# Kernel tuning notes

Measured on AMD Instinct MI355X. Metric: run time of the kernel, lower is better.

## Reference

```python
import jax, jax.numpy as jnp
import numpy as np

B = 8192       # n_cells per batch
G = 512        # n_genes
D = 64         # expression latent dim


def setup_inputs() -> dict:
    key = jax.random.key(0)
    k1, k2 = jax.random.split(key)
    velocity = jax.random.normal(k1, (B, G), dtype=jnp.float32)
    expression_latent = jax.random.normal(k2, (B, D), dtype=jnp.float32)
    return {"velocity": velocity, "expression_latent": expression_latent}


def reference(velocity, expression_latent):
    # weighted_diff[i, j] = sum_g (v_i[g] - v_j[g])^2
    # computed via the Gram trick: ||v_i||^2 + ||v_j||^2 - 2 v_i . v_j
    # (same math as materializing the (B, B, G) diff tensor and summing over g)
    sq_norm = jnp.sum(velocity * velocity, axis=1)              # [B]
    gram = jnp.einsum('ig,jg->ij', velocity, velocity)          # [B, B]
    weighted_diff = sq_norm[:, None] + sq_norm[None, :] - 2.0 * gram  # [B, B]

    # row-softmax of latent similarity matrix
    sim_logits = jnp.einsum('id,jd->ij', expression_latent, expression_latent)  # [B, B]
    expression_similarity = jax.nn.softmax(sim_logits, axis=1)

    batch_size = velocity.shape[0]
    tangent_loss = jnp.sum(expression_similarity * weighted_diff) / (batch_size * batch_size)
    return tangent_loss
```

## Files before the change

kernel.cpp:

```cpp
#include <hip/hip_runtime.h>


#define SEL_T 32.0f

typedef _Float16 half8 __attribute__((ext_vector_type(8)));
typedef float    f32x4 __attribute__((ext_vector_type(4)));
typedef long     l2t   __attribute__((ext_vector_type(2)));

#define MFMA16(a, b, c) __builtin_amdgcn_mfma_f32_16x16x32_f16(a, b, c, 0, 0, 0)
#define MFMA8(a, b, c)  __builtin_amdgcn_mfma_f32_16x16x32_fp8_fp8(a, b, c, 0, 0, 0)

__global__ __launch_bounds__(256) void k_prep(
    const float* __restrict__ V, const float* __restrict__ E,
    float* __restrict__ n, float* __restrict__ ne,
    float* __restrict__ Z, float* __restrict__ num,
    unsigned char* __restrict__ VF8, _Float16* __restrict__ EFh,
    unsigned* __restrict__ cnt) {
    int rt = blockIdx.x;
    int tid = threadIdx.x, wave = tid >> 6, lane = tid & 63;
    if (rt == 0 && tid == 0) *cnt = 0;
    int m = lane >> 2, q = lane & 3;
    int row = rt * 16 + m;
    const float* vr = V + (size_t)row * 512;
    float sn = 0.f;
#pragma unroll
    for (int it = 0; it < 2; ++it) {
        int c = wave + it * 4;
        const float4* p0 = (const float4*)(vr + c * 64 + q * 8);
        const float4* p1 = (const float4*)(vr + c * 64 + 32 + q * 8);
        float4 a0 = p0[0], a1 = p0[1], b0 = p1[0], b1 = p1[1];
        int w0 = 0, w1 = 0, w2 = 0, w3 = 0;
        w0 = __builtin_amdgcn_cvt_pk_fp8_f32(a0.x, a0.y, w0, false);
        w0 = __builtin_amdgcn_cvt_pk_fp8_f32(a0.z, a0.w, w0, true);
        w1 = __builtin_amdgcn_cvt_pk_fp8_f32(a1.x, a1.y, w1, false);
        w1 = __builtin_amdgcn_cvt_pk_fp8_f32(a1.z, a1.w, w1, true);
        w2 = __builtin_amdgcn_cvt_pk_fp8_f32(b0.x, b0.y, w2, false);
        w2 = __builtin_amdgcn_cvt_pk_fp8_f32(b0.z, b0.w, w2, true);
        w3 = __builtin_amdgcn_cvt_pk_fp8_f32(b1.x, b1.y, w3, false);
        w3 = __builtin_amdgcn_cvt_pk_fp8_f32(b1.z, b1.w, w3, true);
        uint4 o;
        o.x = (unsigned)w0; o.y = (unsigned)w1;
        o.z = (unsigned)w2; o.w = (unsigned)w3;
        *(uint4*)(VF8 + (((size_t)rt * 8 + c) << 10) + lane * 16) = o;
        sn += a0.x*a0.x + a0.y*a0.y + a0.z*a0.z + a0.w*a0.w
            + a1.x*a1.x + a1.y*a1.y + a1.z*a1.z + a1.w*a1.w
            + b0.x*b0.x + b0.y*b0.y + b0.z*b0.z + b0.w*b0.w
            + b1.x*b1.x + b1.y*b1.y + b1.z*b1.z + b1.w*b1.w;
    }
    __shared__ float sred[4][64];
    sred[wave][lane] = sn;
    __syncthreads();
    if (tid < 16) {
        float s = 0.f;
#pragma unroll
        for (int w = 0; w < 4; ++w)
#pragma unroll
            for (int qq = 0; qq < 4; ++qq) s += sred[w][tid * 4 + qq];
        int rr = rt * 16 + tid;
        n[rr] = s;
        Z[rr] = 1.0f;
        num[rr] = 0.0f;
    }
    if (tid < 128) {
        int rl = tid >> 3, u = tid & 7;
        int erow = rt * 16 + rl;
        const float4* er = (const float4*)(E + (size_t)erow * 64);
        float4 x0 = er[u * 2], x1 = er[u * 2 + 1];
        float xf[8] = {x0.x, x0.y, x0.z, x0.w, x1.x, x1.y, x1.z, x1.w};
        half8 h;
        float se = 0.f;
#pragma unroll
        for (int k = 0; k < 8; ++k) {
            h[k] = (_Float16)xf[k];
            se += xf[k] * xf[k];
        }
        int kc = u >> 2, qq = u & 3;
        *(half8*)(EFh + ((size_t)rt * 2 + kc) * 512 + rl * 32 + qq * 8) = h;
        se += __shfl_xor(se, 1, 64);
        se += __shfl_xor(se, 2, 64);
        se += __shfl_xor(se, 4, 64);
        if (u == 0) ne[erow] = se;
    }
}

__global__ __launch_bounds__(256, 3) void k_mega(
    const unsigned char* __restrict__ VF8, const _Float16* __restrict__ EFh,
    const float* __restrict__ ne, const float* __restrict__ nrm,
    float* __restrict__ Z, float* __restrict__ num) {
    int blk0 = blockIdx.x;
    int blk = (blk0 & 7) * 260 + (blk0 >> 3);
    int by = (int)((sqrtf(8.f * (float)blk + 1.f) - 1.f) * 0.5f);
    while ((by + 1) * (by + 2) / 2 <= blk) ++by;
    while (by * (by + 1) / 2 > blk) --by;
    int bx = blk - by * (by + 1) / 2;
    int i0 = bx << 7, j0 = by << 7;
    bool diag = (bx == by);

    __shared__ float sNeI[128], sNeJ[128], sNI[128], sNJ[128];
    __shared__ float scr[1024];

    int tid = threadIdx.x;
    if (tid < 128) { sNeI[tid] = ne[i0 + tid]; sNI[tid] = nrm[i0 + tid]; }
    else { sNeJ[tid - 128] = ne[j0 + tid - 128]; sNJ[tid - 128] = nrm[j0 + tid - 128]; }
    __syncthreads();

    int wave = tid >> 6, lane = tid & 63;
    int m = lane & 15, quad = lane >> 4;
    int wi = wave & 1, wj = wave >> 1;
    int rtA = (i0 >> 4) + wi * 4;
    int rtB = (j0 >> 4) + wj * 4;
    size_t loH = (size_t)(m * 32 + quad * 8);
    size_t loB = (size_t)(m * 64 + quad * 16);

    f32x4 gacc[4][4] = {};
    for (int c = 0; c < 8; ++c) {
        l2t a[4], b[4];
#pragma unroll
        for (int im = 0; im < 4; ++im)
            a[im] = *(const l2t*)(VF8 + (((size_t)(rtA + im) * 8 + c) << 10) + loB);
#pragma unroll
        for (int jn = 0; jn < 4; ++jn)
            b[jn] = *(const l2t*)(VF8 + (((size_t)(rtB + jn) * 8 + c) << 10) + loB);
#pragma unroll
        for (int jn = 0; jn < 4; ++jn)
#pragma unroll
            for (int im = 0; im < 4; ++im) {
                gacc[im][jn] = MFMA8(a[im][0], b[jn][0], gacc[im][jn]);
                gacc[im][jn] = MFMA8(a[im][1], b[jn][1], gacc[im][jn]);
            }
    }

    half8 bh[4][2];
#pragma unroll
    for (int jn = 0; jn < 4; ++jn) {
        size_t bb = (size_t)(rtB + jn) * 2 * 512 + loH;
        bh[jn][0] = *(const half8*)(EFh + bb);
        bh[jn][1] = *(const half8*)(EFh + bb + 512);
    }
    float zj[4] = {}, nj_[4] = {};
#pragma unroll
    for (int im = 0; im < 4; ++im) {
        size_t ab = (size_t)(rtA + im) * 2 * 512 + loH;
        half8 ah0 = *(const half8*)(EFh + ab);
        half8 ah1 = *(const half8*)(EFh + ab + 512);
        f32x4 zi4 = {0.f, 0.f, 0.f, 0.f};
        f32x4 ni4 = {0.f, 0.f, 0.f, 0.f};
#pragma unroll
        for (int jn = 0; jn < 4; ++jn) {
            f32x4 acc = {0.f, 0.f, 0.f, 0.f};
            acc = MFMA16(ah0, bh[jn][0], acc);
            acc = MFMA16(ah1, bh[jn][1], acc);
            int jl = (wj << 6) + jn * 16 + m;
            int jg = j0 + jl;
            float nej = sNeJ[jl], nnj = sNJ[jl];
            f32x4 g4 = gacc[im][jn];
            bool p[4];
            bool anyp = false;
#pragma unroll
            for (int r = 0; r < 4; ++r) {
                int il = (wi << 6) + im * 16 + quad * 4 + r;
                int ig = i0 + il;
                float nei = sNeI[il];
                p[r] = (acc[r] > fminf(nei, nej) - SEL_T) && (!diag || ig < jg);
                anyp |= p[r];
            }
            if (__builtin_amdgcn_ballot_w64(anyp)) {
#pragma unroll
                for (int r = 0; r < 4; ++r) {
                    if (p[r]) {
                        int il = (wi << 6) + im * 16 + quad * 4 + r;
                        float nei = sNeI[il], nni = sNI[il];
                        float s = acc[r];
                        float wiw = __expf(s - nei);
                        float wjw = __expf(s - nej);
                        float wd = nni + nnj - 2.f * g4[r];
                        zi4[r] += wiw;  ni4[r] += wiw * wd;
                        zj[jn] += wjw;  nj_[jn] += wjw * wd;
                    }
                }
            }
        }
#pragma unroll
        for (int msk = 1; msk < 16; msk <<= 1) {
#pragma unroll
            for (int r = 0; r < 4; ++r) {
                zi4[r] += __shfl_xor(zi4[r], msk, 64);
                ni4[r] += __shfl_xor(ni4[r], msk, 64);
            }
        }
        if (m == 0) {
            int row0 = (wi << 6) + im * 16 + quad * 4;
            *(f32x4*)(scr + (wj << 7) + row0)       = zi4;
            *(f32x4*)(scr + 256 + (wj << 7) + row0) = ni4;
        }
    }
#pragma unroll
    for (int msk = 16; msk < 64; msk <<= 1) {
#pragma unroll
        for (int jn = 0; jn < 4; ++jn) {
            zj[jn]  += __shfl_xor(zj[jn],  msk, 64);
            nj_[jn] += __shfl_xor(nj_[jn], msk, 64);
        }
    }
    if (quad == 0) {
#pragma unroll
        for (int jn = 0; jn < 4; ++jn) {
            int jl = (wj << 6) + jn * 16 + m;
            scr[512 + (wi << 7) + jl] = zj[jn];
            scr[768 + (wi << 7) + jl] = nj_[jn];
        }
    }
    __syncthreads();
    if (tid < 128) {
        float az = scr[tid]       + scr[128 + tid];
        float an = scr[256 + tid] + scr[384 + tid];
        if (az != 0.f || an != 0.f) {
            atomicAdd(Z + i0 + tid,   az);
            atomicAdd(num + i0 + tid, an);
        }
    } else {
        int cidx = tid - 128;
        float az = scr[512 + cidx] + scr[640 + cidx];
        float an = scr[768 + cidx] + scr[896 + cidx];
        if (az != 0.f || an != 0.f) {
            atomicAdd(Z + j0 + cidx,   az);
            atomicAdd(num + j0 + cidx, an);
        }
    }
}

__global__ __launch_bounds__(256) void k_red(
    const float* __restrict__ Z, const float* __restrict__ num,
    double* __restrict__ part, unsigned* __restrict__ cnt,
    float* __restrict__ out) {
    int r = (blockIdx.x << 8) + threadIdx.x;
    __shared__ double sd[256];
    sd[threadIdx.x] = (double)num[r] / (double)Z[r];
    __syncthreads();
    for (int st = 128; st > 0; st >>= 1) {
        if (threadIdx.x < st) sd[threadIdx.x] += sd[threadIdx.x + st];
        __syncthreads();
    }
    if (threadIdx.x == 0) {
        part[blockIdx.x] = sd[0];
        __threadfence();
        unsigned old = atomicAdd(cnt, 1u);
        if (old == 31u) {
            __threadfence();
            double a = 0.0;
            for (int k = 0; k < 32; ++k) a += part[k];
            out[0] = (float)(a / 67108864.0);
        }
    }
}

extern "C" void kernel_launch(void* const* d_in, const int* in_sizes, int n_in,
                              void* d_out, int out_size, void* d_ws, size_t ws_size,
                              hipStream_t stream) {
    const float* V = (const float*)d_in[0];
    const float* E = (const float*)d_in[1];
    float* out = (float*)d_out;
    char* ws = (char*)d_ws;

    float*         n_   = (float*)(ws + 0);
    float*         ne   = (float*)(ws + 32768);
    float*         Z    = (float*)(ws + 65536);
    float*         num  = (float*)(ws + 98304);
    unsigned char* VF8  = (unsigned char*)(ws + 131072);
    _Float16*      EFh  = (_Float16*)(ws + 4325376);
    double*        part = (double*)(ws + 5373952);
    unsigned*      cnt  = (unsigned*)(ws + 5374208);

    k_prep<<<512, 256, 0, stream>>>(V, E, n_, ne, Z, num, VF8, EFh, cnt);
    k_mega<<<2080, 256, 0, stream>>>(VF8, EFh, ne, n_, Z, num);
    k_red <<<32, 256, 0, stream>>>(Z, num, part, cnt, out);
}
```

Before: 134.8 us.

## Fuse final reduction into mega kernel, supertile block order, stagger K chunks

Removes the separate reduction kernel: the last block to finish, detected with an atomic counter, reads Z and num and reduces them in place, saving a launch and a dependent kernel boundary. Triangular block indexing now walks 8x8 super-tiles so concurrently running blocks share i/j row tiles in cache. Each wave starts its K-chunk loop at a different offset to spread memory accesses. The cost is a tail where one block does the final reduction serially, plus extra fences and atomics at the end of every block.

```diff
diff --git a/kernel.cpp b/kernel.cpp
--- a/kernel.cpp
+++ b/kernel.cpp
@@ -86,18 +86,35 @@
 __global__ __launch_bounds__(256, 3) void k_mega(
     const unsigned char* __restrict__ VF8, const _Float16* __restrict__ EFh,
     const float* __restrict__ ne, const float* __restrict__ nrm,
-    float* __restrict__ Z, float* __restrict__ num) {
+    float* __restrict__ Z, float* __restrict__ num,
+    unsigned* __restrict__ cnt, float* __restrict__ out) {
     int blk0 = blockIdx.x;
-    int blk = (blk0 & 7) * 260 + (blk0 >> 3);
-    int by = (int)((sqrtf(8.f * (float)blk + 1.f) - 1.f) * 0.5f);
-    while ((by + 1) * (by + 2) / 2 <= blk) ++by;
-    while (by * (by + 1) / 2 > blk) --by;
-    int bx = blk - by * (by + 1) / 2;
+    int g = (blk0 & 7) * 260 + (blk0 >> 3);
+    int SY = 0;
+#pragma unroll
+    for (int s = 1; s < 8; ++s) if (32 * s * s + 4 * s <= g) SY = s;
+    int rr = g - (32 * SY * SY + 4 * SY);
+    int bx, by;
+    if (rr < 64 * SY) {
+        int SX = rr >> 6, t = rr & 63;
+        bx = (SX << 3) + (t & 7);
+        by = (SY << 3) + (t >> 3);
+    } else {
+        int t = rr - 64 * SY;
+        int ly = 0;
+#pragma unroll
+        for (int s = 1; s < 8; ++s) if (s * (s + 1) / 2 <= t) ly = s;
+        int lx = t - ly * (ly + 1) / 2;
+        bx = (SY << 3) + lx;
+        by = (SY << 3) + ly;
+    }
     int i0 = bx << 7, j0 = by << 7;
     bool diag = (bx == by);
 
     __shared__ float sNeI[128], sNeJ[128], sNI[128], sNJ[128];
     __shared__ float scr[1024];
+    __shared__ double sd[256];
+    __shared__ unsigned sLast;
 
     int tid = threadIdx.x;
     if (tid < 128) { sNeI[tid] = ne[i0 + tid]; sNI[tid] = nrm[i0 + tid]; }
@@ -113,7 +130,9 @@
     size_t loB = (size_t)(m * 64 + quad * 16);
 
     f32x4 gacc[4][4] = {};
-    for (int c = 0; c < 8; ++c) {
+    int cbase = wave << 1;
+    for (int cc = 0; cc < 8; ++cc) {
+        int c = (cc + cbase) & 7;
         l2t a[4], b[4];
 #pragma unroll
         for (int im = 0; im < 4; ++im)
@@ -227,30 +246,28 @@
             atomicAdd(num + j0 + cidx, an);
         }
     }
-}
-
-__global__ __launch_bounds__(256) void k_red(
-    const float* __restrict__ Z, const float* __restrict__ num,
-    double* __restrict__ part, unsigned* __restrict__ cnt,
-    float* __restrict__ out) {
-    int r = (blockIdx.x << 8) + threadIdx.x;
-    __shared__ double sd[256];
-    sd[threadIdx.x] = (double)num[r] / (double)Z[r];
-    __syncthreads();
-    for (int st = 128; st > 0; st >>= 1) {
-        if (threadIdx.x < st) sd[threadIdx.x] += sd[threadIdx.x + st];
+
+    __syncthreads();
+    if (tid == 0) {
+        __threadfence();
+        sLast = (atomicAdd(cnt, 1u) == 2079u) ? 1u : 0u;
+    }
+    __syncthreads();
+    if (sLast) {
+        __threadfence();
+        double acc = 0.0;
+        for (int r = tid; r < 8192; r += 256) {
+            float zz = __hip_atomic_load(Z + r,   __ATOMIC_RELAXED, __HIP_MEMORY_SCOPE_AGENT);
+            float nn = __hip_atomic_load(num + r, __ATOMIC_RELAXED, __HIP_MEMORY_SCOPE_AGENT);
+            acc += (double)nn / (double)zz;
+        }
+        sd[tid] = acc;
         __syncthreads();
-    }
-    if (threadIdx.x == 0) {
-        part[blockIdx.x] = sd[0];
-        __threadfence();
-        unsigned old = atomicAdd(cnt, 1u);
-        if (old == 31u) {
-            __threadfence();
-            double a = 0.0;
-            for (int k = 0; k < 32; ++k) a += part[k];
-            out[0] = (float)(a / 67108864.0);
-        }
+        for (int st = 128; st > 0; st >>= 1) {
+            if (tid < st) sd[tid] += sd[tid + st];
+            __syncthreads();
+        }
+        if (tid == 0) out[0] = (float)(sd[0] / 67108864.0);
     }
 }
 
@@ -268,10 +285,8 @@
     float*         num  = (float*)(ws + 98304);
     unsigned char* VF8  = (unsigned char*)(ws + 131072);
     _Float16*      EFh  = (_Float16*)(ws + 4325376);
-    double*        part = (double*)(ws + 5373952);
     unsigned*      cnt  = (unsigned*)(ws + 5374208);
 
     k_prep<<<512, 256, 0, stream>>>(V, E, n_, ne, Z, num, VF8, EFh, cnt);
-    k_mega<<<2080, 256, 0, stream>>>(VF8, EFh, ne, n_, Z, num);
-    k_red <<<32, 256, 0, stream>>>(Z, num, part, cnt, out);
+    k_mega<<<2080, 256, 0, stream>>>(VF8, EFh, ne, n_, Z, num, cnt, out);
 }
```

New measurement: 162.1 us. 1.2x slower.
